# Optimization experiments

Hardware: AMD Instinct MI355X
Metric: run time of the kernel (lower is better)

Reference implementation:

```python
import jax, jax.numpy as jnp
import numpy as np

B, S, D = 4, 2048, 256


def setup_inputs() -> dict:
    key = jax.random.key(0)
    ks = jax.random.split(key, 8)
    context = jax.random.normal(ks[0], (B, S, D), dtype=jnp.float32)
    eos_mask = jax.random.randint(ks[1], (B, S, S), 0, 2, dtype=jnp.int32)
    prior = jax.random.uniform(ks[2], (B, S, S), dtype=jnp.float32)
    Wq = jax.random.normal(ks[3], (D, D), dtype=jnp.float32) * 0.02
    bq = jnp.zeros((D,), dtype=jnp.float32)
    Wk = jax.random.normal(ks[4], (D, D), dtype=jnp.float32) * 0.02
    bk = jnp.zeros((D,), dtype=jnp.float32)
    ln_a = jnp.ones((D,), dtype=jnp.float32)
    ln_b = jnp.zeros((D,), dtype=jnp.float32)
    return {"context": context, "prior": prior, "Wq": Wq, "bq": bq,
            "Wk": Wk, "bk": bk, "ln_a": ln_a, "ln_b": ln_b,
            "eos_mask": eos_mask}


def reference(context, prior, Wq, bq, Wk, bk, ln_a, ln_b, eos_mask):
    seq = context.shape[1]
    # LayerNorm (torch: unbiased std, eps added to std)
    mean = context.mean(axis=-1, keepdims=True)
    std = jnp.std(context, axis=-1, ddof=1, keepdims=True)
    x = ln_a * (context - mean) / (std + 1e-6) + ln_b

    idx = jnp.arange(seq)
    diff = idx[None, :] - idx[:, None]
    a = diff == 1                      # superdiagonal
    offdiag = jnp.abs(diff) == 1       # a + c (super + sub diagonal)
    eye = diff == 0                    # b
    tri = jnp.triu(jnp.ones((seq, seq), dtype=jnp.float32))

    # mask = eos_mask & (a + c)  (precedence: & binds looser than +)
    mask = jnp.bitwise_and(eos_mask, offdiag.astype(jnp.int32))

    # torch Linear: y = x @ W.T + b
    query = x @ Wq.T + bq
    key = x @ Wk.T + bk
    scores = jnp.einsum('bqd,bkd->bqk', query, key) / 256.0
    scores = jnp.where(mask == 0, -1e9, scores)
    neibor = jax.nn.softmax(scores, axis=-1)
    neibor = jnp.sqrt(neibor * neibor.transpose(0, 2, 1) + 1e-9)
    neibor = prior + (1.0 - prior) * neibor

    # log -> zero except superdiagonal -> triangular matmul -> exp
    t = jnp.where(a, jnp.log(neibor + 1e-9), 0.0) @ tri   # [B,S,S]
    g = jnp.exp(jnp.matmul(tri, t))                        # [B,S,S]
    strict_upper = jnp.logical_and(tri.astype(bool), jnp.logical_not(eye))
    g = jnp.where(strict_upper, g, 0.0)  # masked_fill(tri - b == 0, 0)
    g = g + g.transpose(0, 2, 1) + jnp.where(eye, neibor, 1e-9)
    return g
```

## Files before the change

### kernel.cpp

```cpp
#include <hip/hip_runtime.h>
#include <math.h>

#define SS 2048
#define DD 256
#define NB 4
#define NR (NB * SS)

__global__ __launch_bounds__(256) void prep_kernel(
    const float* __restrict__ Wq, const float* __restrict__ Wk,
    const float* __restrict__ bq, float* __restrict__ A, float* __restrict__ u) {
    int t = threadIdx.x;
    int d = blockIdx.x;
    if (d < DD) {
        float acc = 0.0f;
        for (int i = 0; i < DD; i++) acc += Wq[i * DD + d] * Wk[i * DD + t];
        A[d * DD + t] = acc;
    } else {
        float acc = 0.0f;
        for (int i = 0; i < DD; i++) acc += Wk[i * DD + t] * bq[i];
        u[t] = acc;
    }
}

__global__ __launch_bounds__(256) void ln_kernel(
    const float4* __restrict__ ctx4, const float4* __restrict__ ln_a4,
    const float4* __restrict__ ln_b4, float4* __restrict__ xn4) {
    int lane = threadIdx.x & 63;
    int wave = threadIdx.x >> 6;
    int r = blockIdx.x * 4 + wave;
    float4 v = ctx4[(size_t)r * 64 + lane];
    float s = v.x + v.y + v.z + v.w;
#pragma unroll
    for (int off = 32; off > 0; off >>= 1) s += __shfl_xor(s, off, 64);
    float mean = s * (1.0f / 256.0f);
    float4 d = make_float4(v.x - mean, v.y - mean, v.z - mean, v.w - mean);
    float s2 = d.x * d.x + d.y * d.y + d.z * d.z + d.w * d.w;
#pragma unroll
    for (int off = 32; off > 0; off >>= 1) s2 += __shfl_xor(s2, off, 64);
    float inv = 1.0f / (sqrtf(s2 * (1.0f / 255.0f)) + 1e-6f);
    float4 ga = ln_a4[lane], gb = ln_b4[lane];
    xn4[(size_t)r * 64 + lane] = make_float4(
        ga.x * d.x * inv + gb.x, ga.y * d.y * inv + gb.y,
        ga.z * d.z * inv + gb.z, ga.w * d.w * inv + gb.w);
}

#define BK 32
#define FMA4(accv, a, bv) \
    accv.x += (a) * bv.x; accv.y += (a) * bv.y; \
    accv.z += (a) * bv.z; accv.w += (a) * bv.w;

__global__ __launch_bounds__(256) void gemm_score_kernel(
    const float* __restrict__ X, const float* __restrict__ A,
    const float* __restrict__ u, const int* __restrict__ eos,
    float4* __restrict__ pvals) {
    __shared__ float Xs[BK][33];
    __shared__ float As[BK][256];
    int tid = threadIdx.x;
    int tx = tid & 15, ty = tid >> 4;
    int row0 = blockIdx.x * 32;
    const float4* X4 = (const float4*)X;
    const float4* A4 = (const float4*)A;

    float4 acc[2][4] = {};
    for (int k0 = 0; k0 < DD; k0 += BK) {
        {
            int m = tid >> 3;
            int kq = (tid & 7) * 4;
            float4 x4 = X4[(size_t)(row0 + m) * 64 + (k0 >> 2) + (tid & 7)];
            Xs[kq + 0][m] = x4.x; Xs[kq + 1][m] = x4.y;
            Xs[kq + 2][m] = x4.z; Xs[kq + 3][m] = x4.w;
        }
#pragma unroll
        for (int q = 0; q < 8; q++) {
            int f4 = q * 256 + tid;
            int k = f4 >> 6, c4 = f4 & 63;
            *(float4*)&As[k][c4 * 4] = A4[(size_t)(k0 + k) * 64 + c4];
        }
        __syncthreads();
#pragma unroll
        for (int k = 0; k < BK; k++) {
            float a0 = Xs[k][ty * 2];
            float a1 = Xs[k][ty * 2 + 1];
            float4 b0 = *(const float4*)&As[k][tx * 4];
            float4 b1 = *(const float4*)&As[k][tx * 4 + 64];
            float4 b2 = *(const float4*)&As[k][tx * 4 + 128];
            float4 b3 = *(const float4*)&As[k][tx * 4 + 192];
            FMA4(acc[0][0], a0, b0) FMA4(acc[0][1], a0, b1)
            FMA4(acc[0][2], a0, b2) FMA4(acc[0][3], a0, b3)
            FMA4(acc[1][0], a1, b0) FMA4(acc[1][1], a1, b1)
            FMA4(acc[1][2], a1, b2) FMA4(acc[1][3], a1, b3)
        }
        __syncthreads();
    }
    const float4* u4 = (const float4*)u;
#pragma unroll
    for (int q = 0; q < 4; q++) {
        float4 uv = u4[q * 16 + tx];
        acc[0][q].x += uv.x; acc[0][q].y += uv.y; acc[0][q].z += uv.z; acc[0][q].w += uv.w;
        acc[1][q].x += uv.x; acc[1][q].y += uv.y; acc[1][q].z += uv.z; acc[1][q].w += uv.w;
    }
    const float4* xn4 = (const float4*)X;
#pragma unroll
    for (int i = 0; i < 2; i++) {
        int r = row0 + ty * 2 + i;
        int s = r & (SS - 1), b = r >> 11;
        bool has_n = (s < SS - 1), has_p = (s > 0);
        float partial = 0.0f;
#pragma unroll
        for (int q = 0; q < 4; q++) {
            float4 wn = has_n ? xn4[(size_t)(r + 1) * 64 + q * 16 + tx]
                              : make_float4(0, 0, 0, 0);
            float4 wp = has_p ? xn4[(size_t)(r - 1) * 64 + q * 16 + tx]
                              : make_float4(0, 0, 0, 0);
            partial += acc[i][q].x * (wn.x - wp.x) + acc[i][q].y * (wn.y - wp.y)
                     + acc[i][q].z * (wn.z - wp.z) + acc[i][q].w * (wn.w - wp.w);
        }
#pragma unroll
        for (int off = 8; off > 0; off >>= 1) partial += __shfl_xor(partial, off, 64);
        if (tx == 0) {
            size_t base = (size_t)b * SS * SS + (size_t)s * SS;
            bool mn = has_n && (eos[base + s + 1] != 0);
            bool mp = has_p && (eos[base + s - 1] != 0);
            float pn, pp, pd;
            if (mn && mp) {
                float d = partial * (1.0f / 256.0f);
                pn = 1.0f / (1.0f + __expf(-d));
                pp = 1.0f - pn;
                pd = 0.0f;
            } else if (mn) { pn = 1.0f; pp = 0.0f; pd = 0.0f; }
            else if (mp)   { pn = 0.0f; pp = 1.0f; pd = 0.0f; }
            else           { pn = pp = pd = (1.0f / 2048.0f); }
            pvals[r] = make_float4(pn, pp, pd, 0.0f);
        }
    }
}

__global__ __launch_bounds__(256) void scan_kernel(
    const float4* __restrict__ pvals, const float* __restrict__ prior,
    float* __restrict__ P) {
    int b = blockIdx.x, t = threadIdx.x;
    int base_s = t * 8;
    double loc[8];
    double run = 0.0;
#pragma unroll
    for (int i = 0; i < 8; i++) {
        loc[i] = run;
        int s = base_s + i;
        float lv = 0.0f;
        if (s < SS - 1) {
            int r = b * SS + s;
            float4 pv = pvals[r];
            float4 pv1 = pvals[r + 1];
            float ns = sqrtf(pv.x * pv1.y + 1e-9f);
            float pr = prior[(size_t)b * SS * SS + (size_t)s * SS + s + 1];
            float neib = pr + (1.0f - pr) * ns;
            lv = logf(neib + 1e-9f);
        }
        run += (double)lv;
    }
    int lane = t & 63, wave = t >> 6;
    double v = run;
#pragma unroll
    for (int off = 1; off < 64; off <<= 1) {
        double uu = __shfl_up(v, off, 64);
        if (lane >= off) v += uu;
    }
    __shared__ double wsum[4];
    if (lane == 63) wsum[wave] = v;
    __syncthreads();
    double woff = 0.0;
    for (int w = 0; w < wave; w++) woff += wsum[w];
    double texcl = woff + (v - run);
#pragma unroll
    for (int i = 0; i < 8; i++)
        P[b * SS + base_s + i] = (float)(texcl + loc[i]);
}

__global__ __launch_bounds__(256) void fill_kernel(
    const float* __restrict__ P, const float4* __restrict__ pvals,
    const float* __restrict__ prior, float* __restrict__ out) {
    int blk = blockIdx.x;
    int i = blk & (SS - 1), b = blk >> 11;
    int t = threadIdx.x;
    __shared__ float shPi, shDv;
    if (t == 0) {
        shPi = P[blk];
        float pd = pvals[blk].z;
        float prd = prior[(size_t)b * SS * SS + (size_t)i * SS + i];
        shDv = prd + (1.0f - prd) * sqrtf(pd * pd + 1e-9f);
    }
    __syncthreads();
    float Pi = shPi, dv = shDv;
    const float* Pb = P + b * SS;
    size_t outbase = (size_t)blk * SS;
    float4 pj0 = *(const float4*)(Pb + t * 8);
    float4 pj1 = *(const float4*)(Pb + t * 8 + 4);
    float pj[8] = {pj0.x, pj0.y, pj0.z, pj0.w, pj1.x, pj1.y, pj1.z, pj1.w};
    float res[8];
#pragma unroll
    for (int k = 0; k < 8; k++) {
        int j = t * 8 + k;
        float d = (j > i) ? (pj[k] - Pi) : (Pi - pj[k]);
        float val = __expf(d) + 1e-9f;
        res[k] = (j == i) ? dv : val;
    }
    *(float4*)(out + outbase + t * 8) = make_float4(res[0], res[1], res[2], res[3]);
    *(float4*)(out + outbase + t * 8 + 4) = make_float4(res[4], res[5], res[6], res[7]);
}

extern "C" void kernel_launch(void* const* d_in, const int* in_sizes, int n_in,
                              void* d_out, int out_size, void* d_ws, size_t ws_size,
                              hipStream_t stream) {
    const float* context = (const float*)d_in[0];
    const float* prior   = (const float*)d_in[1];
    const float* Wq      = (const float*)d_in[2];
    const float* bq      = (const float*)d_in[3];
    const float* Wk      = (const float*)d_in[4];
    const float* ln_a    = (const float*)d_in[6];
    const float* ln_b    = (const float*)d_in[7];
    const int*   eos     = (const int*)d_in[8];
    float* out = (float*)d_out;

    float* ws = (float*)d_ws;
    float* xn    = ws;
    float* A     = ws + 4194304;
    float* u     = ws + 4259840;
    float4* pv   = (float4*)(ws + 4260096);
    float* P     = ws + 4292864;

    prep_kernel<<<DD + 1, 256, 0, stream>>>(Wq, Wk, bq, A, u);
    ln_kernel<<<NR / 4, 256, 0, stream>>>((const float4*)context,
                                          (const float4*)ln_a,
                                          (const float4*)ln_b, (float4*)xn);
    gemm_score_kernel<<<NR / 32, 256, 0, stream>>>(xn, A, u, eos, pv);
    scan_kernel<<<NB, 256, 0, stream>>>(pv, prior, P);
    fill_kernel<<<NR, 256, 0, stream>>>(P, pv, prior, out);
}
```

Before: 220.5 us.

## Fuse LayerNorm into the score GEMM kernel with shared-memory halo rows

Removes the separate LayerNorm kernel. Each GEMM block now normalises its 32 rows plus one halo row on each side directly into shared memory and reads neighbour rows from there. This drops one launch, the write and reread of the normalised 8 MB activation, and the global neighbour loads. In exchange the kernel uses more shared memory (34x260 floats), which may lower occupancy, and the 2-row halo is normalised redundantly across blocks.

```diff
diff --git a/kernel.cpp b/kernel.cpp
--- a/kernel.cpp
+++ b/kernel.cpp
@@ -22,54 +22,49 @@
     }
 }
 
-__global__ __launch_bounds__(256) void ln_kernel(
-    const float4* __restrict__ ctx4, const float4* __restrict__ ln_a4,
-    const float4* __restrict__ ln_b4, float4* __restrict__ xn4) {
-    int lane = threadIdx.x & 63;
-    int wave = threadIdx.x >> 6;
-    int r = blockIdx.x * 4 + wave;
-    float4 v = ctx4[(size_t)r * 64 + lane];
-    float s = v.x + v.y + v.z + v.w;
-#pragma unroll
-    for (int off = 32; off > 0; off >>= 1) s += __shfl_xor(s, off, 64);
-    float mean = s * (1.0f / 256.0f);
-    float4 d = make_float4(v.x - mean, v.y - mean, v.z - mean, v.w - mean);
-    float s2 = d.x * d.x + d.y * d.y + d.z * d.z + d.w * d.w;
-#pragma unroll
-    for (int off = 32; off > 0; off >>= 1) s2 += __shfl_xor(s2, off, 64);
-    float inv = 1.0f / (sqrtf(s2 * (1.0f / 255.0f)) + 1e-6f);
-    float4 ga = ln_a4[lane], gb = ln_b4[lane];
-    xn4[(size_t)r * 64 + lane] = make_float4(
-        ga.x * d.x * inv + gb.x, ga.y * d.y * inv + gb.y,
-        ga.z * d.z * inv + gb.z, ga.w * d.w * inv + gb.w);
-}
-
 #define BK 32
+#define XP 260
 #define FMA4(accv, a, bv) \
     accv.x += (a) * bv.x; accv.y += (a) * bv.y; \
     accv.z += (a) * bv.z; accv.w += (a) * bv.w;
 
 __global__ __launch_bounds__(256) void gemm_score_kernel(
-    const float* __restrict__ X, const float* __restrict__ A,
+    const float4* __restrict__ ctx4, const float4* __restrict__ ln_a4,
+    const float4* __restrict__ ln_b4, const float* __restrict__ A,
     const float* __restrict__ u, const int* __restrict__ eos,
     float4* __restrict__ pvals) {
-    __shared__ float Xs[BK][33];
+    __shared__ float Xn[34][XP];
     __shared__ float As[BK][256];
     int tid = threadIdx.x;
+    int lane = tid & 63;
+    int wave = tid >> 6;
+    int row0 = blockIdx.x * 32;
+    const float4* A4 = (const float4*)A;
+
+    float4 ga = ln_a4[lane], gb = ln_b4[lane];
+    for (int rr = wave; rr < 34; rr += 4) {
+        int g = row0 - 1 + rr;
+        g = (g < 0) ? 0 : (g > NR - 1 ? NR - 1 : g);
+        float4 v = ctx4[(size_t)g * 64 + lane];
+        float s = v.x + v.y + v.z + v.w;
+#pragma unroll
+        for (int off = 32; off > 0; off >>= 1) s += __shfl_xor(s, off, 64);
+        float mean = s * (1.0f / 256.0f);
+        float4 dd = make_float4(v.x - mean, v.y - mean, v.z - mean, v.w - mean);
+        float s2 = dd.x * dd.x + dd.y * dd.y + dd.z * dd.z + dd.w * dd.w;
+#pragma unroll
+        for (int off = 32; off > 0; off >>= 1) s2 += __shfl_xor(s2, off, 64);
+        float inv = 1.0f / (sqrtf(s2 * (1.0f / 255.0f)) + 1e-6f);
+        float* xr = &Xn[rr][lane * 4];
+        xr[0] = ga.x * dd.x * inv + gb.x;
+        xr[1] = ga.y * dd.y * inv + gb.y;
+        xr[2] = ga.z * dd.z * inv + gb.z;
+        xr[3] = ga.w * dd.w * inv + gb.w;
+    }
+
     int tx = tid & 15, ty = tid >> 4;
-    int row0 = blockIdx.x * 32;
-    const float4* X4 = (const float4*)X;
-    const float4* A4 = (const float4*)A;
-
     float4 acc[2][4] = {};
     for (int k0 = 0; k0 < DD; k0 += BK) {
-        {
-            int m = tid >> 3;
-            int kq = (tid & 7) * 4;
-            float4 x4 = X4[(size_t)(row0 + m) * 64 + (k0 >> 2) + (tid & 7)];
-            Xs[kq + 0][m] = x4.x; Xs[kq + 1][m] = x4.y;
-            Xs[kq + 2][m] = x4.z; Xs[kq + 3][m] = x4.w;
-        }
 #pragma unroll
         for (int q = 0; q < 8; q++) {
             int f4 = q * 256 + tid;
@@ -79,8 +74,8 @@
         __syncthreads();
 #pragma unroll
         for (int k = 0; k < BK; k++) {
-            float a0 = Xs[k][ty * 2];
-            float a1 = Xs[k][ty * 2 + 1];
+            float a0 = Xn[1 + ty * 2][k0 + k];
+            float a1 = Xn[2 + ty * 2][k0 + k];
             float4 b0 = *(const float4*)&As[k][tx * 4];
             float4 b1 = *(const float4*)&As[k][tx * 4 + 64];
             float4 b2 = *(const float4*)&As[k][tx * 4 + 128];
@@ -99,21 +94,23 @@
         acc[0][q].x += uv.x; acc[0][q].y += uv.y; acc[0][q].z += uv.z; acc[0][q].w += uv.w;
         acc[1][q].x += uv.x; acc[1][q].y += uv.y; acc[1][q].z += uv.z; acc[1][q].w += uv.w;
     }
-    const float4* xn4 = (const float4*)X;
 #pragma unroll
     for (int i = 0; i < 2; i++) {
+        int li = 1 + ty * 2 + i;
         int r = row0 + ty * 2 + i;
         int s = r & (SS - 1), b = r >> 11;
         bool has_n = (s < SS - 1), has_p = (s > 0);
+        float fn = has_n ? 1.0f : 0.0f, fp = has_p ? 1.0f : 0.0f;
         float partial = 0.0f;
 #pragma unroll
         for (int q = 0; q < 4; q++) {
-            float4 wn = has_n ? xn4[(size_t)(r + 1) * 64 + q * 16 + tx]
-                              : make_float4(0, 0, 0, 0);
-            float4 wp = has_p ? xn4[(size_t)(r - 1) * 64 + q * 16 + tx]
-                              : make_float4(0, 0, 0, 0);
-            partial += acc[i][q].x * (wn.x - wp.x) + acc[i][q].y * (wn.y - wp.y)
-                     + acc[i][q].z * (wn.z - wp.z) + acc[i][q].w * (wn.w - wp.w);
+            int c = q * 64 + tx * 4;
+            float wx = fn * Xn[li + 1][c + 0] - fp * Xn[li - 1][c + 0];
+            float wy = fn * Xn[li + 1][c + 1] - fp * Xn[li - 1][c + 1];
+            float wz = fn * Xn[li + 1][c + 2] - fp * Xn[li - 1][c + 2];
+            float ww = fn * Xn[li + 1][c + 3] - fp * Xn[li - 1][c + 3];
+            partial += acc[i][q].x * wx + acc[i][q].y * wy
+                     + acc[i][q].z * wz + acc[i][q].w * ww;
         }
 #pragma unroll
         for (int off = 8; off > 0; off >>= 1) partial += __shfl_xor(partial, off, 64);
@@ -222,17 +219,15 @@
     float* out = (float*)d_out;
 
     float* ws = (float*)d_ws;
-    float* xn    = ws;
-    float* A     = ws + 4194304;
-    float* u     = ws + 4259840;
-    float4* pv   = (float4*)(ws + 4260096);
-    float* P     = ws + 4292864;
+    float* A     = ws;
+    float* u     = ws + 65536;
+    float4* pv   = (float4*)(ws + 65792);
+    float* P     = ws + 98560;
 
     prep_kernel<<<DD + 1, 256, 0, stream>>>(Wq, Wk, bq, A, u);
-    ln_kernel<<<NR / 4, 256, 0, stream>>>((const float4*)context,
-                                          (const float4*)ln_a,
-                                          (const float4*)ln_b, (float4*)xn);
-    gemm_score_kernel<<<NR / 32, 256, 0, stream>>>(xn, A, u, eos, pv);
+    gemm_score_kernel<<<NR / 32, 256, 0, stream>>>(
+        (const float4*)context, (const float4*)ln_a, (const float4*)ln_b,
+        A, u, eos, pv);
     scan_kernel<<<NB, 256, 0, stream>>>(pv, prior, P);
     fill_kernel<<<NR, 256, 0, stream>>>(P, pv, prior, out);
 }
```

After: 219.8 us. About the same (-0.3%).
